# Performance work log

Measured on AMD Instinct MI355X. Metric: run time of the kernel, lower is better.

The kernel has to match this reference:

```python
import jax, jax.numpy as jnp
import numpy as np

N_NODES = 50000
N_EDGES = 600000
D_IN = 256    # hidden_lstm
D_GNN = 128   # hidden_gnn
D_OUT = 1     # out_channels


def setup_inputs() -> dict:
    key = jax.random.key(0)
    ks = jax.random.split(key, 8)
    x = jax.random.normal(ks[0], (N_NODES, D_IN), dtype=jnp.float32)
    edge_index = jax.random.randint(ks[1], (2, N_EDGES), 0, N_NODES, dtype=jnp.int32)
    # SAGEConv params: lin_l applied to aggregated neighbors (with bias), lin_r to root
    s_in = 1.0 / np.sqrt(D_IN)
    W_l = jax.random.uniform(ks[2], (D_IN, D_GNN), jnp.float32, -s_in, s_in)
    b_l = jax.random.uniform(ks[3], (D_GNN,), jnp.float32, -s_in, s_in)
    W_r = jax.random.uniform(ks[4], (D_IN, D_GNN), jnp.float32, -s_in, s_in)
    # fc head
    s_g = 1.0 / np.sqrt(D_GNN)
    W_fc = jax.random.uniform(ks[5], (D_GNN, D_OUT), jnp.float32, -s_g, s_g)
    b_fc = jax.random.uniform(ks[6], (D_OUT,), jnp.float32, -s_g, s_g)
    return {"x": x, "edge_index": edge_index, "W_l": W_l, "b_l": b_l,
            "W_r": W_r, "W_fc": W_fc, "b_fc": b_fc}


def reference(x, edge_index, W_l, b_l, W_r, W_fc, b_fc):
    # SAGEConv, aggr='mean': out = lin_l(mean_{j in N(i)} x_j) + lin_r(x_i)
    src = edge_index[0]  # message source
    dst = edge_index[1]  # message target
    n = x.shape[0]
    agg = jax.ops.segment_sum(x[src], dst, num_segments=n)            # [N, D_IN]
    cnt = jax.ops.segment_sum(jnp.ones((src.shape[0], 1), x.dtype), dst,
                              num_segments=n)                         # [N, 1]
    mean = agg / jnp.maximum(cnt, 1.0)
    h = mean @ W_l + b_l + x @ W_r                                    # [N, D_GNN]
    pred = jax.nn.sigmoid(h @ W_fc + b_fc).squeeze()                  # [N]
    return h, pred
```

## Files before the change

### kernel.cpp

```cpp
#include <hip/hip_runtime.h>
#include <hip/hip_bf16.h>
#include <math.h>

#define N_NODES 50000
#define N_EDGES 600000
#define D_IN 256
#define D_GNN 128
#define CAP 32
#define MAX_OVER 8192
#define CSTRIDE 16

typedef short s16x8 __attribute__((ext_vector_type(8)));
typedef float f32x4 __attribute__((ext_vector_type(4)));

__device__ __forceinline__ unsigned short f2bf(float f) {
  unsigned int u = __float_as_uint(f);
  u += 0x7FFFu + ((u >> 16) & 1u);
  return (unsigned short)(u >> 16);
}

__global__ __launch_bounds__(256) void pack0(
    const float* __restrict__ Wl, const float* __restrict__ Wr,
    ushort* __restrict__ Wcp, int* __restrict__ cursor,
    int* __restrict__ ovcnt) {
  int i = blockIdx.x * 256 + threadIdx.x;
  if (i < N_NODES * CSTRIDE) cursor[i] = 0;
  if (i == 0) ovcnt[0] = 0;
  if (i < 8192) {
    int q = i & 3, col = (i >> 2) & 255, ks = i >> 10;
    const float* W = (col < 128) ? Wl : Wr;
    int c = col & 127;
    int k0 = ks * 32 + q * 8;
    s16x8 v;
#pragma unroll
    for (int j = 0; j < 8; j++) v[j] = (short)f2bf(W[(k0 + j) * D_GNN + c]);
    *((s16x8*)(Wcp + (size_t)i * 8)) = v;
  }
}

__global__ __launch_bounds__(512, 4) void fused_gemm_fill(
    const float* __restrict__ x, const ushort* __restrict__ Wcp,
    const float* __restrict__ b_l, const int* __restrict__ ei,
    int* __restrict__ cursor, ushort* __restrict__ colp,
    int* __restrict__ ovcnt, int2* __restrict__ over,
    ushort* __restrict__ yb, ushort* __restrict__ yrb) {
  __shared__ float xs[64 * 256];
  const int t = threadIdx.x;
  const int n0 = blockIdx.x * 64;
  const int l = t & 63;
  const int w = t >> 6;

#pragma unroll
  for (int j = 0; j < 8; j++) {
    const int row = j * 8 + w;
    int gn = n0 + row;
    if (gn >= N_NODES) gn = N_NODES - 1;
    const int sc = (l & ~7) | ((l & 7) ^ (row & 7));
    __builtin_amdgcn_global_load_lds(
        (const __attribute__((address_space(1))) unsigned int*)(
            x + (size_t)gn * 256 + sc * 4),
        (__attribute__((address_space(3))) unsigned int*)(xs + row * 256),
        16, 0, 0);
  }

  {
    const int stride = gridDim.x * 512;
    for (int e = blockIdx.x * 512 + t; e < N_EDGES; e += stride) {
      int src = ei[e];
      int dst = ei[N_EDGES + e];
      int pos = atomicAdd(&cursor[dst * CSTRIDE], 1);
      if (pos < CAP) {
        colp[dst * CAP + pos] = (ushort)src;
      } else {
        int o = atomicAdd(ovcnt, 1);
        if (o < MAX_OVER) over[o] = make_int2(dst, src);
      }
    }
  }

  const int wrow = w & 1;
  const int wcol = w >> 1;
  const int lq = l >> 4, l16 = l & 15;

  f32x4 acc[2][4];
#pragma unroll
  for (int a = 0; a < 2; a++)
#pragma unroll
    for (int b = 0; b < 4; b++) acc[a][b] = (f32x4){0.f, 0.f, 0.f, 0.f};

  const float* ap0[2];
  const float* ap1[2];
#pragma unroll
  for (int nt = 0; nt < 2; nt++) {
    int rl = wrow * 32 + nt * 16 + l16;
    int o0 = (lq * 2) ^ (rl & 7);
    ap0[nt] = xs + rl * 256 + o0 * 4;
    ap1[nt] = xs + rl * 256 + (o0 ^ 1) * 4;
  }
  const ushort* bptr[4];
#pragma unroll
  for (int ct = 0; ct < 4; ct++) {
    int col = wcol * 64 + ct * 16 + l16;
    bptr[ct] = Wcp + ((size_t)col * 4 + lq) * 8;
  }

  s16x8 B[4], Bn[4];
#pragma unroll
  for (int ct = 0; ct < 4; ct++) B[ct] = *((const s16x8*)(bptr[ct]));

  __syncthreads();

  union { s16x8 v; ushort4 u[2]; } ua;
#pragma unroll
  for (int ks = 0; ks < 8; ks++) {
    s16x8 A[2];
#pragma unroll
    for (int nt = 0; nt < 2; nt++) {
      float4 a0 = *((const float4*)(ap0[nt] + ks * 32));
      float4 a1 = *((const float4*)(ap1[nt] + ks * 32));
      __hip_bfloat162 h0 = __float22bfloat162_rn(make_float2(a0.x, a0.y));
      __hip_bfloat162 h1 = __float22bfloat162_rn(make_float2(a0.z, a0.w));
      __hip_bfloat162 h2 = __float22bfloat162_rn(make_float2(a1.x, a1.y));
      __hip_bfloat162 h3 = __float22bfloat162_rn(make_float2(a1.z, a1.w));
      ua.u[0].x = ((ushort2*)&h0)->x; ua.u[0].y = ((ushort2*)&h0)->y;
      ua.u[0].z = ((ushort2*)&h1)->x; ua.u[0].w = ((ushort2*)&h1)->y;
      ua.u[1].x = ((ushort2*)&h2)->x; ua.u[1].y = ((ushort2*)&h2)->y;
      ua.u[1].z = ((ushort2*)&h3)->x; ua.u[1].w = ((ushort2*)&h3)->y;
      A[nt] = ua.v;
    }
    if (ks < 7) {
#pragma unroll
      for (int ct = 0; ct < 4; ct++)
        Bn[ct] = *((const s16x8*)(bptr[ct] + (size_t)(ks + 1) * 256 * 32));
    }
#pragma unroll
    for (int nt = 0; nt < 2; nt++)
#pragma unroll
      for (int ct = 0; ct < 4; ct++)
        acc[nt][ct] = __builtin_amdgcn_mfma_f32_16x16x32_bf16(
            A[nt], B[ct], acc[nt][ct], 0, 0, 0);
#pragma unroll
    for (int ct = 0; ct < 4; ct++) B[ct] = Bn[ct];
  }

  __syncthreads();
  ushort* eb = (ushort*)xs;
#pragma unroll
  for (int nt = 0; nt < 2; nt++) {
#pragma unroll
    for (int ct = 0; ct < 4; ct++) {
      int col = wcol * 64 + ct * 16 + l16;
      float bias = (col >= 128) ? b_l[col - 128] : 0.f;
#pragma unroll
      for (int r = 0; r < 4; r++) {
        int rl = wrow * 32 + nt * 16 + lq * 4 + r;
        eb[rl * 264 + col] = f2bf(acc[nt][ct][r] + bias);
      }
    }
  }
  __syncthreads();
#pragma unroll
  for (int p = 0; p < 4; p++) {
    int id2 = p * 512 + t;
    int rl = id2 >> 5;
    int c8 = (id2 & 31) * 8;
    int gn = n0 + rl;
    if (gn < N_NODES) {
      s16x8 v = *((const s16x8*)(eb + rl * 264 + c8));
      if (c8 < 128)
        *((s16x8*)(yb + (size_t)gn * D_GNN + c8)) = v;
      else
        *((s16x8*)(yrb + (size_t)gn * D_GNN + (c8 - 128))) = v;
    }
  }
}

__global__ __launch_bounds__(256) void gather_pred(
    const int* __restrict__ cursor, const ushort* __restrict__ colp,
    const int* __restrict__ ovcnt, const int2* __restrict__ over,
    const ushort* __restrict__ yb, const ushort* __restrict__ yrb,
    const float* __restrict__ Wfc, const float* __restrict__ bfc,
    float* __restrict__ h, float* __restrict__ pred) {
  const int node = (blockIdx.x * 256 + threadIdx.x) >> 6;
  const int lane = threadIdx.x & 63;
  if (node >= N_NODES) return;
  const int degt = cursor[node * CSTRIDE];
  const int m = min(degt, CAP);
  float ax = 0.f, ay = 0.f;
  const unsigned int* y32 = (const unsigned int*)yb;

  int c = (lane < m) ? (int)colp[node * CAP + lane] : 0;
  int j = 0;
  for (; j + 4 <= m; j += 4) {
    int s0 = __shfl(c, j), s1 = __shfl(c, j + 1);
    int s2 = __shfl(c, j + 2), s3 = __shfl(c, j + 3);
    unsigned int v0 = y32[(size_t)s0 * 64 + lane];
    unsigned int v1 = y32[(size_t)s1 * 64 + lane];
    unsigned int v2 = y32[(size_t)s2 * 64 + lane];
    unsigned int v3 = y32[(size_t)s3 * 64 + lane];
    ax += __uint_as_float(v0 << 16) + __uint_as_float(v1 << 16) +
          __uint_as_float(v2 << 16) + __uint_as_float(v3 << 16);
    ay += __uint_as_float(v0 & 0xFFFF0000u) + __uint_as_float(v1 & 0xFFFF0000u) +
          __uint_as_float(v2 & 0xFFFF0000u) + __uint_as_float(v3 & 0xFFFF0000u);
  }
  for (; j < m; j++) {
    int s0 = __shfl(c, j);
    unsigned int v0 = y32[(size_t)s0 * 64 + lane];
    ax += __uint_as_float(v0 << 16);
    ay += __uint_as_float(v0 & 0xFFFF0000u);
  }
  if (degt > CAP) {
    int nov = min(ovcnt[0], MAX_OVER);
    for (int k = 0; k < nov; k++) {
      int2 ov = over[k];
      if (ov.x == node) {
        unsigned int v0 = y32[(size_t)ov.y * 64 + lane];
        ax += __uint_as_float(v0 << 16);
        ay += __uint_as_float(v0 & 0xFFFF0000u);
      }
    }
  }

  const float ic = degt > 0 ? 1.f / (float)degt : 0.f;
  unsigned int yrv = ((const unsigned int*)yrb)[(size_t)node * 64 + lane];
  float h0 = ax * ic + __uint_as_float(yrv << 16);
  float h1 = ay * ic + __uint_as_float(yrv & 0xFFFF0000u);
  float2 hv; hv.x = h0; hv.y = h1;
  ((float2*)h)[(size_t)node * 64 + lane] = hv;
  float s = h0 * Wfc[2 * lane] + h1 * Wfc[2 * lane + 1];
#pragma unroll
  for (int off = 32; off > 0; off >>= 1) s += __shfl_down(s, off);
  if (lane == 0) pred[node] = 1.f / (1.f + expf(-(s + bfc[0])));
}

extern "C" void kernel_launch(void* const* d_in, const int* in_sizes, int n_in,
                              void* d_out, int out_size, void* d_ws,
                              size_t ws_size, hipStream_t stream) {
  const float* x   = (const float*)d_in[0];
  const int*   ei  = (const int*)d_in[1];
  const float* Wl  = (const float*)d_in[2];
  const float* bl  = (const float*)d_in[3];
  const float* Wr  = (const float*)d_in[4];
  const float* Wfc = (const float*)d_in[5];
  const float* bfc = (const float*)d_in[6];

  float* out  = (float*)d_out;
  float* h    = out;
  float* pred = out + (size_t)N_NODES * D_GNN;

  ushort* Wcp   = (ushort*)d_ws;
  ushort* yb    = Wcp + 8192 * 8;
  ushort* yrb   = yb + (size_t)N_NODES * D_GNN;
  int*   cursor = (int*)(yrb + (size_t)N_NODES * D_GNN);
  int*   ovcnt  = cursor + N_NODES * CSTRIDE;
  int2*  over   = (int2*)(ovcnt + 1);
  ushort* colp  = (ushort*)(over + MAX_OVER);

  pack0<<<(N_NODES * CSTRIDE + 255) / 256, 256, 0, stream>>>(
      Wl, Wr, Wcp, cursor, ovcnt);

  fused_gemm_fill<<<(N_NODES + 63) / 64, 512, 0, stream>>>(
      x, Wcp, bl, ei, cursor, colp, ovcnt, over, yb, yrb);

  gather_pred<<<(N_NODES * 64 + 255) / 256, 256, 0, stream>>>(
      cursor, colp, ovcnt, over, yb, yrb, Wfc, bfc, h, pred);
}
```

Measured before the change: 170.8 us.

## Split edge-fill into dedicated blocks, compact cursor array, unroll gather by eight

Edge CSR filling moves out of every GEMM block into a fixed set of dedicated blocks, with four edges processed per iteration to overlap atomics. The per-node cursor array loses its 16-int padding, which shrinks the zeroing work and memory footprint but may raise atomic contention on shared cache lines. The gather loop gains an 8-wide unroll for more loads in flight. The change gives up the previous overlap of edge filling with the async LDS load in the GEMM blocks.

```diff
diff --git a/kernel.cpp b/kernel.cpp
--- a/kernel.cpp
+++ b/kernel.cpp
@@ -8,7 +8,7 @@
 #define D_GNN 128
 #define CAP 32
 #define MAX_OVER 8192
-#define CSTRIDE 16
+#define EDGE_BLKS 64
 
 typedef short s16x8 __attribute__((ext_vector_type(8)));
 typedef float f32x4 __attribute__((ext_vector_type(4)));
@@ -24,7 +24,7 @@
     ushort* __restrict__ Wcp, int* __restrict__ cursor,
     int* __restrict__ ovcnt) {
   int i = blockIdx.x * 256 + threadIdx.x;
-  if (i < N_NODES * CSTRIDE) cursor[i] = 0;
+  if (i < N_NODES) cursor[i] = 0;
   if (i == 0) ovcnt[0] = 0;
   if (i < 8192) {
     int q = i & 3, col = (i >> 2) & 255, ks = i >> 10;
@@ -46,7 +46,39 @@
     ushort* __restrict__ yb, ushort* __restrict__ yrb) {
   __shared__ float xs[64 * 256];
   const int t = threadIdx.x;
-  const int n0 = blockIdx.x * 64;
+
+  if (blockIdx.x < EDGE_BLKS) {
+    const int stride = EDGE_BLKS * 512;
+    int e = blockIdx.x * 512 + t;
+    for (; e + 3 * stride < N_EDGES; e += 4 * stride) {
+      int s0 = ei[e],              d0 = ei[N_EDGES + e];
+      int s1 = ei[e + stride],     d1 = ei[N_EDGES + e + stride];
+      int s2 = ei[e + 2 * stride], d2 = ei[N_EDGES + e + 2 * stride];
+      int s3 = ei[e + 3 * stride], d3 = ei[N_EDGES + e + 3 * stride];
+      int p0 = atomicAdd(&cursor[d0], 1);
+      int p1 = atomicAdd(&cursor[d1], 1);
+      int p2 = atomicAdd(&cursor[d2], 1);
+      int p3 = atomicAdd(&cursor[d3], 1);
+      if (p0 < CAP) colp[d0 * CAP + p0] = (ushort)s0;
+      else { int o = atomicAdd(ovcnt, 1); if (o < MAX_OVER) over[o] = make_int2(d0, s0); }
+      if (p1 < CAP) colp[d1 * CAP + p1] = (ushort)s1;
+      else { int o = atomicAdd(ovcnt, 1); if (o < MAX_OVER) over[o] = make_int2(d1, s1); }
+      if (p2 < CAP) colp[d2 * CAP + p2] = (ushort)s2;
+      else { int o = atomicAdd(ovcnt, 1); if (o < MAX_OVER) over[o] = make_int2(d2, s2); }
+      if (p3 < CAP) colp[d3 * CAP + p3] = (ushort)s3;
+      else { int o = atomicAdd(ovcnt, 1); if (o < MAX_OVER) over[o] = make_int2(d3, s3); }
+    }
+    for (; e < N_EDGES; e += stride) {
+      int src = ei[e];
+      int dst = ei[N_EDGES + e];
+      int pos = atomicAdd(&cursor[dst], 1);
+      if (pos < CAP) colp[dst * CAP + pos] = (ushort)src;
+      else { int o = atomicAdd(ovcnt, 1); if (o < MAX_OVER) over[o] = make_int2(dst, src); }
+    }
+    return;
+  }
+
+  const int n0 = (blockIdx.x - EDGE_BLKS) * 64;
   const int l = t & 63;
   const int w = t >> 6;
 
@@ -61,21 +93,6 @@
             x + (size_t)gn * 256 + sc * 4),
         (__attribute__((address_space(3))) unsigned int*)(xs + row * 256),
         16, 0, 0);
-  }
-
-  {
-    const int stride = gridDim.x * 512;
-    for (int e = blockIdx.x * 512 + t; e < N_EDGES; e += stride) {
-      int src = ei[e];
-      int dst = ei[N_EDGES + e];
-      int pos = atomicAdd(&cursor[dst * CSTRIDE], 1);
-      if (pos < CAP) {
-        colp[dst * CAP + pos] = (ushort)src;
-      } else {
-        int o = atomicAdd(ovcnt, 1);
-        if (o < MAX_OVER) over[o] = make_int2(dst, src);
-      }
-    }
   }
 
   const int wrow = w & 1;
@@ -184,13 +201,35 @@
   const int node = (blockIdx.x * 256 + threadIdx.x) >> 6;
   const int lane = threadIdx.x & 63;
   if (node >= N_NODES) return;
-  const int degt = cursor[node * CSTRIDE];
+  const int degt = cursor[node];
   const int m = min(degt, CAP);
   float ax = 0.f, ay = 0.f;
   const unsigned int* y32 = (const unsigned int*)yb;
 
   int c = (lane < m) ? (int)colp[node * CAP + lane] : 0;
   int j = 0;
+  for (; j + 8 <= m; j += 8) {
+    int s0 = __shfl(c, j),     s1 = __shfl(c, j + 1);
+    int s2 = __shfl(c, j + 2), s3 = __shfl(c, j + 3);
+    int s4 = __shfl(c, j + 4), s5 = __shfl(c, j + 5);
+    int s6 = __shfl(c, j + 6), s7 = __shfl(c, j + 7);
+    unsigned int v0 = y32[(size_t)s0 * 64 + lane];
+    unsigned int v1 = y32[(size_t)s1 * 64 + lane];
+    unsigned int v2 = y32[(size_t)s2 * 64 + lane];
+    unsigned int v3 = y32[(size_t)s3 * 64 + lane];
+    unsigned int v4 = y32[(size_t)s4 * 64 + lane];
+    unsigned int v5 = y32[(size_t)s5 * 64 + lane];
+    unsigned int v6 = y32[(size_t)s6 * 64 + lane];
+    unsigned int v7 = y32[(size_t)s7 * 64 + lane];
+    ax += __uint_as_float(v0 << 16) + __uint_as_float(v1 << 16) +
+          __uint_as_float(v2 << 16) + __uint_as_float(v3 << 16) +
+          __uint_as_float(v4 << 16) + __uint_as_float(v5 << 16) +
+          __uint_as_float(v6 << 16) + __uint_as_float(v7 << 16);
+    ay += __uint_as_float(v0 & 0xFFFF0000u) + __uint_as_float(v1 & 0xFFFF0000u) +
+          __uint_as_float(v2 & 0xFFFF0000u) + __uint_as_float(v3 & 0xFFFF0000u) +
+          __uint_as_float(v4 & 0xFFFF0000u) + __uint_as_float(v5 & 0xFFFF0000u) +
+          __uint_as_float(v6 & 0xFFFF0000u) + __uint_as_float(v7 & 0xFFFF0000u);
+  }
   for (; j + 4 <= m; j += 4) {
     int s0 = __shfl(c, j), s1 = __shfl(c, j + 1);
     int s2 = __shfl(c, j + 2), s3 = __shfl(c, j + 3);
@@ -252,14 +291,13 @@
   ushort* yb    = Wcp + 8192 * 8;
   ushort* yrb   = yb + (size_t)N_NODES * D_GNN;
   int*   cursor = (int*)(yrb + (size_t)N_NODES * D_GNN);
-  int*   ovcnt  = cursor + N_NODES * CSTRIDE;
+  int*   ovcnt  = cursor + N_NODES;
   int2*  over   = (int2*)(ovcnt + 1);
   ushort* colp  = (ushort*)(over + MAX_OVER);
 
-  pack0<<<(N_NODES * CSTRIDE + 255) / 256, 256, 0, stream>>>(
-      Wl, Wr, Wcp, cursor, ovcnt);
-
-  fused_gemm_fill<<<(N_NODES + 63) / 64, 512, 0, stream>>>(
+  pack0<<<(N_NODES + 255) / 256, 256, 0, stream>>>(Wl, Wr, Wcp, cursor, ovcnt);
+
+  fused_gemm_fill<<<EDGE_BLKS + (N_NODES + 63) / 64, 512, 0, stream>>>(
       x, Wcp, bl, ei, cursor, colp, ovcnt, over, yb, yrb);
 
   gather_pred<<<(N_NODES * 64 + 255) / 256, 256, 0, stream>>>(
```

Measured after the change: 178.0 us. 4.2% more time.
